# Kernel optimization log

Measured on AMD Instinct MI355X. Metric: run time of the kernel, lower is better.

The kernel has to match this reference:

```python
import jax, jax.numpy as jnp
import numpy as np
import math

D = 256; H = 8; DH = 32; FF = 2048; L = 6; B = 4; S = 1022


def _pe(n, d):
    pos = np.arange(n)[:, None]
    div = np.exp(np.arange(0, d, 2) * (-math.log(10000.0) / d))
    pe = np.zeros((n, d), np.float32)
    pe[:, 0::2] = np.sin(pos * div)
    pe[:, 1::2] = np.cos(pos * div)
    return jnp.asarray(pe)


def _ln(x, g, b):
    mu = x.mean(-1, keepdims=True)
    v = ((x - mu) ** 2).mean(-1, keepdims=True)
    return (x - mu) / jnp.sqrt(v + 1e-5) * g + b


def _forward(x, cls1, cls2, Wqkv, bqkv, Wo, bo, ln1_g, ln1_b, W1, b1, W2, b2, ln2_g, ln2_b, idx, pad):
    n = x.shape[1] + 2  # insert cls1 and cls2 tokens
    h = jnp.stack([jnp.concatenate([cls1, x[i, :idx[i]], cls2, x[i, idx[i]:]], axis=0) for i in range(B)])
    h = h + _pe(n, D)[None]  # [B,N,D]
    # block-diagonal two-segment mask per sample (additive bias form)
    pos = np.arange(n)
    bias = []
    for i in range(B):
        v1 = pos <= idx[i]
        v2 = (pos > idx[i]) & (pos < n - pad[i])
        allowed = np.outer(v1, v1) | np.outer(v2, v2)
        bias.append(np.where(allowed, 0.0, -1e9).astype(np.float32))
    bias = jnp.asarray(np.stack(bias))[:, None]  # [B,1,N,N]
    scale = 1.0 / math.sqrt(DH)
    for l in range(L):
        qkv = h @ Wqkv[l].T + bqkv[l]  # [B,N,3D]
        q, k, v = jnp.split(qkv, 3, axis=-1)
        q = q.reshape(B, n, H, DH).transpose(0, 2, 1, 3)
        k = k.reshape(B, n, H, DH).transpose(0, 2, 1, 3)
        v = v.reshape(B, n, H, DH).transpose(0, 2, 1, 3)
        scores = jnp.einsum('bhqd,bhkd->bhqk', q, k) * scale + bias
        p = jax.nn.softmax(scores, axis=-1)
        a = jnp.einsum('bhqk,bhkd->bhqd', p, v).transpose(0, 2, 1, 3).reshape(B, n, D)
        h = _ln(h + a @ Wo[l].T + bo[l], ln1_g[l], ln1_b[l])
        ff = jax.nn.relu(h @ W1[l].T + b1[l]) @ W2[l].T + b2[l]
        h = _ln(h + ff, ln2_g[l], ln2_b[l])
    # cls token outputs: position 0 (cls1) and position idx+1 (cls2)
    return jnp.stack([jnp.stack([h[i, 0], h[i, idx[i] + 1]]) for i in range(B)])  # [4,2,256]


def setup_inputs():
    key = jax.random.key(0)
    ks = jax.random.split(key, 8)
    s = 0.02
    return {
        'x': jax.random.normal(ks[0], (B, S, D), jnp.float32),
        'mask': jnp.zeros((1,), jnp.bool_),  # unused by the original forward
        'indices': jnp.array([[500, 600, 400, 300], [0, 0, 0, 0]], jnp.int32),
        'cls1': jax.random.uniform(ks[1], (1, D), jnp.float32),
        'cls2': jax.random.uniform(ks[2], (1, D), jnp.float32),
        'Wqkv': jax.random.normal(ks[3], (L, 3 * D, D), jnp.float32) * s,
        'bqkv': jnp.zeros((L, 3 * D), jnp.float32),
        'Wo': jax.random.normal(ks[4], (L, D, D), jnp.float32) * s,
        'bo': jnp.zeros((L, D), jnp.float32),
        'ln1_g': jnp.ones((L, D), jnp.float32),
        'ln1_b': jnp.zeros((L, D), jnp.float32),
        'W1': jax.random.normal(ks[5], (L, FF, D), jnp.float32) * s,
        'b1': jnp.zeros((L, FF), jnp.float32),
        'W2': jax.random.normal(ks[6], (L, D, FF), jnp.float32) * s,
        'b2': jnp.zeros((L, D), jnp.float32),
        'ln2_g': jnp.ones((L, D), jnp.float32),
        'ln2_b': jnp.zeros((L, D), jnp.float32),
    }


def reference(x, mask, indices, cls1, cls2, Wqkv, bqkv, Wo, bo, ln1_g, ln1_b, W1, b1, W2, b2, ln2_g, ln2_b):
    ind = np.asarray(indices)
    idx = [int(t) for t in ind[0]]
    pad = [int(t) for t in ind[1]]
    return _forward(x, cls1, cls2, Wqkv, bqkv, Wo, bo, ln1_g, ln1_b, W1, b1, W2, b2, ln2_g, ln2_b, idx, pad)
```

## Files before the change

### kernel.cpp

```cpp
#include <hip/hip_runtime.h>
#include <hip/hip_bf16.h>
#include <math.h>

typedef __hip_bfloat16 bf16;
typedef short bf16x8 __attribute__((ext_vector_type(8)));
typedef short short4v __attribute__((ext_vector_type(4)));
typedef float f32x4 __attribute__((ext_vector_type(4)));

#define D_MODEL 256
#define NTOK 1024
#define SEQ 1022
#define BATCH 4
#define NLAYER 6

__device__ inline void gload_lds16(const void* g, void* l) {
    __builtin_amdgcn_global_load_lds(
        (const __attribute__((address_space(1))) void*)g,
        (__attribute__((address_space(3))) void*)l, 16, 0, 0);
}

__global__ __launch_bounds__(256) void cast_kernel(
    const float* __restrict__ in, bf16* __restrict__ out, int n)
{
    int i = (blockIdx.x * 256 + threadIdx.x) * 4;
    if (i >= n) return;
    f32x4 v = *(const f32x4*)(in + i);
    out[i + 0] = __float2bfloat16(v[0]);
    out[i + 1] = __float2bfloat16(v[1]);
    out[i + 2] = __float2bfloat16(v[2]);
    out[i + 3] = __float2bfloat16(v[3]);
}

__global__ __launch_bounds__(256) void embed_kernel(
    const float* __restrict__ x, const float* __restrict__ cls1,
    const float* __restrict__ cls2, const int* __restrict__ ind,
    float* __restrict__ h, bf16* __restrict__ hb)
{
    int i = blockIdx.x * 256 + threadIdx.x;
    int d = i & 255;
    int pos = (i >> 8) & 1023;
    int b = i >> 18;
    int idx = ind[b];
    float v;
    if (pos == 0) v = cls1[d];
    else if (pos == idx + 1) v = cls2[d];
    else if (pos <= idx) v = x[(b * SEQ + pos - 1) * D_MODEL + d];
    else v = x[(b * SEQ + pos - 2) * D_MODEL + d];
    int p = d >> 1;
    float freq = expf(-(float)p * (logf(10000.0f) / 128.0f));
    float ang = (float)pos * freq;
    v += (d & 1) ? cosf(ang) : sinf(ang);
    h[i] = v;
    hb[i] = __float2bfloat16(v);
}

template<int MR, int NR, int RELU, int HAS_RES, int WF32, int WBF16, int WVT>
__global__ __launch_bounds__(256) void mfma_gemm(
    const bf16* __restrict__ A, const bf16* __restrict__ W,
    const float* __restrict__ bias, const float* __restrict__ R,
    float* __restrict__ Cf, bf16* __restrict__ Cb, bf16* __restrict__ vTb,
    int M, int N, int K)
{
    constexpr int BM = MR * 32, BN = NR * 32;
    constexpr int ACH = BM * 4;
    constexpr int BCH = BN * 4;
    __shared__ bf16 As[2][BM * 32];
    __shared__ bf16 Bs[2][BN * 32];
    const int ntile = N / BN;
    const int bx = blockIdx.x % ntile, by = blockIdx.x / ntile;
    const int row0 = by * BM, col0 = bx * BN;
    const int tid = threadIdx.x, lane = tid & 63, wave = tid >> 6;
    const int wr = wave >> 1, wc = wave & 1;
    const int l15 = lane & 15, l4 = lane >> 4;

    f32x4 acc[MR][NR];
    #pragma unroll
    for (int m = 0; m < MR; ++m)
        #pragma unroll
        for (int n = 0; n < NR; ++n) acc[m][n] = (f32x4)0.0f;

    const int nk = K / 32;

    auto stage = [&](int buf, int t) {
        const int k0 = t * 32;
        #pragma unroll
        for (int p = 0; p < ACH / 256; ++p) {
            const int cbase = p * 256 + wave * 64;
            const int chunk = cbase + lane;
            const int r = chunk >> 2, c = chunk & 3;
            gload_lds16(A + (size_t)(row0 + r) * K + k0 + c * 8, &As[buf][cbase * 8]);
        }
        #pragma unroll
        for (int p = 0; p < BCH / 256; ++p) {
            const int cbase = p * 256 + wave * 64;
            const int chunk = cbase + lane;
            const int r = chunk >> 2, c = chunk & 3;
            gload_lds16(W + (size_t)(col0 + r) * K + k0 + c * 8, &Bs[buf][cbase * 8]);
        }
    };

    stage(0, 0);
    __syncthreads();
    int cur = 0;
    for (int t = 0; t < nk; ++t) {
        if (t + 1 < nk) stage(cur ^ 1, t + 1);
        bf16x8 af[MR], bfr[NR];
        #pragma unroll
        for (int m = 0; m < MR; ++m)
            af[m] = *(const bf16x8*)&As[cur][(wr * MR * 16 + m * 16 + l15) * 32 + l4 * 8];
        #pragma unroll
        for (int n = 0; n < NR; ++n)
            bfr[n] = *(const bf16x8*)&Bs[cur][(wc * NR * 16 + n * 16 + l15) * 32 + l4 * 8];
        #pragma unroll
        for (int m = 0; m < MR; ++m)
            #pragma unroll
            for (int n = 0; n < NR; ++n)
                acc[m][n] = __builtin_amdgcn_mfma_f32_16x16x32_bf16(af[m], bfr[n], acc[m][n], 0, 0, 0);
        __syncthreads();
        cur ^= 1;
    }

    #pragma unroll
    for (int m = 0; m < MR; ++m) {
        #pragma unroll
        for (int n = 0; n < NR; ++n) {
            const int col = col0 + wc * NR * 16 + n * 16 + l15;
            const float bv = bias[col];
            #pragma unroll
            for (int r = 0; r < 4; ++r) {
                const int row = row0 + wr * MR * 16 + m * 16 + l4 * 4 + r;
                float v = acc[m][n][r] + bv;
                if (HAS_RES) v += R[(size_t)row * N + col];
                if (RELU) v = fmaxf(v, 0.0f);
                if (WF32) Cf[(size_t)row * N + col] = v;
                if (WBF16) {
                    if (WVT && col >= 512) {
                        const int hh = (col >> 5) - 16, d = col & 31;
                        const int bb = row >> 10, tt = row & 1023;
                        vTb[(((size_t)bb * 8 + hh) * 32 + d) * 1024 + tt] = __float2bfloat16(v);
                    } else {
                        Cb[(size_t)row * N + col] = __float2bfloat16(v);
                    }
                }
            }
        }
    }
}

template<int K>
__global__ __launch_bounds__(256) void gemm256_ln_kernel(
    const bf16* __restrict__ A, const bf16* __restrict__ W,
    const float* __restrict__ bias, const float* __restrict__ g,
    const float* __restrict__ be, float* __restrict__ h, bf16* __restrict__ hb)
{
    constexpr int KW = K / 4;
    constexpr int NSTEP = KW / 32;
    __shared__ float part[4][16][260];
    const int tid = threadIdx.x, lane = tid & 63, wave = tid >> 6;
    const int l15 = lane & 15, l4 = lane >> 4;
    const int row0 = blockIdx.x * 16;
    const int kbase = wave * KW;

    f32x4 acc[16];
    #pragma unroll
    for (int n = 0; n < 16; ++n) acc[n] = (f32x4)0.0f;

    #pragma unroll
    for (int s = 0; s < NSTEP; ++s) {
        const int kk = kbase + s * 32;
        const bf16x8 af = *(const bf16x8*)(A + (size_t)(row0 + l15) * K + kk + l4 * 8);
        #pragma unroll
        for (int n = 0; n < 16; ++n) {
            const bf16x8 bf_ = *(const bf16x8*)(W + (size_t)(n * 16 + l15) * K + kk + l4 * 8);
            acc[n] = __builtin_amdgcn_mfma_f32_16x16x32_bf16(af, bf_, acc[n], 0, 0, 0);
        }
    }
    #pragma unroll
    for (int n = 0; n < 16; ++n)
        #pragma unroll
        for (int r = 0; r < 4; ++r)
            part[wave][l4 * 4 + r][n * 16 + l15] = acc[n][r];
    __syncthreads();

    const int row = tid >> 4, colg = tid & 15;
    f32x4 v[4];
    #pragma unroll
    for (int e = 0; e < 4; ++e) {
        v[e] = *(const f32x4*)&part[0][row][colg * 16 + e * 4];
        #pragma unroll
        for (int w = 1; w < 4; ++w)
            v[e] += *(const f32x4*)&part[w][row][colg * 16 + e * 4];
    }
    float* hrow = h + (size_t)(row0 + row) * 256 + colg * 16;
    float s1 = 0.0f;
    #pragma unroll
    for (int e = 0; e < 4; ++e) {
        const f32x4 bv = *(const f32x4*)(bias + colg * 16 + e * 4);
        const f32x4 rv = *(const f32x4*)(hrow + e * 4);
        v[e] += bv + rv;
        s1 += (v[e][0] + v[e][1]) + (v[e][2] + v[e][3]);
    }
    #pragma unroll
    for (int off = 8; off >= 1; off >>= 1) s1 += __shfl_xor(s1, off);
    const float mu = s1 * (1.0f / 256.0f);
    float s2 = 0.0f;
    #pragma unroll
    for (int e = 0; e < 4; ++e) {
        #pragma unroll
        for (int q = 0; q < 4; ++q) { const float d = v[e][q] - mu; s2 += d * d; }
    }
    #pragma unroll
    for (int off = 8; off >= 1; off >>= 1) s2 += __shfl_xor(s2, off);
    const float inv = 1.0f / sqrtf(s2 * (1.0f / 256.0f) + 1e-5f);

    short* hbrow = (short*)hb + (size_t)(row0 + row) * 256 + colg * 16;
    #pragma unroll
    for (int e = 0; e < 4; ++e) {
        const f32x4 gv = *(const f32x4*)(g + colg * 16 + e * 4);
        const f32x4 bv2 = *(const f32x4*)(be + colg * 16 + e * 4);
        f32x4 y;
        short4v pk;
        #pragma unroll
        for (int q = 0; q < 4; ++q) {
            y[q] = (v[e][q] - mu) * inv * gv[q] + bv2[q];
            pk[q] = __builtin_bit_cast(short, __float2bfloat16(y[q]));
        }
        *(f32x4*)(hrow + e * 4) = y;
        *(short4v*)(hbrow + e * 4) = pk;
    }
}

__global__ __launch_bounds__(256) void attn_mfma_kernel(
    const bf16* __restrict__ qkvb, const bf16* __restrict__ vT,
    bf16* __restrict__ att, const int* __restrict__ ind)
{
    __shared__ bf16 Ps[4][16][72];
    const int qt = blockIdx.x & 15;
    const int hh = (blockIdx.x >> 4) & 7;
    const int b  = blockIdx.x >> 7;
    const int idx = ind[b];
    const int segEnd = NTOK - ind[4 + b];
    const int tid = threadIdx.x, lane = tid & 63, wave = tid >> 6;
    const int l15 = lane & 15, l4 = lane >> 4;
    const int q0 = qt * 64 + wave * 16;
    const size_t tokbase = (size_t)b * NTOK;
    const bf16* vTh = vT + (((size_t)b * 8 + hh) * 32) * 1024;
    const float scale = 0.17677669529663687f;

    const bf16x8 qfrag = *(const bf16x8*)(qkvb + (tokbase + q0 + l15) * 768 + hh * 32 + l4 * 8);

    f32x4 acc_o[2];
    acc_o[0] = (f32x4)0.0f; acc_o[1] = (f32x4)0.0f;
    float mrun[4], lrun[4];
    bool v1q[4], v2q[4];
    #pragma unroll
    for (int r = 0; r < 4; ++r) {
        mrun[r] = -1e30f; lrun[r] = 0.0f;
        const int qg = q0 + l4 * 4 + r;
        v1q[r] = (qg <= idx);
        v2q[r] = (qg > idx) && (qg < segEnd);
    }

    const int kbeg = (q0 <= idx) ? 0 : (idx + 1);
    const int kend = (q0 + 15 > idx) ? segEnd : (idx + 1);

    for (int k0 = (kbeg & ~63); k0 < kend; k0 += 64) {
        f32x4 sc[4];
        #pragma unroll
        for (int kt = 0; kt < 4; ++kt) {
            const bf16x8 kf = *(const bf16x8*)
                (qkvb + (tokbase + k0 + kt * 16 + l15) * 768 + 256 + hh * 32 + l4 * 8);
            sc[kt] = __builtin_amdgcn_mfma_f32_16x16x32_bf16(qfrag, kf, (f32x4)0.0f, 0, 0, 0);
        }
        float mloc[4] = {-1e30f, -1e30f, -1e30f, -1e30f};
        #pragma unroll
        for (int kt = 0; kt < 4; ++kt) {
            const int k = k0 + kt * 16 + l15;
            const bool v1k = (k <= idx);
            const bool v2k = (k > idx) && (k < segEnd);
            #pragma unroll
            for (int r = 0; r < 4; ++r) {
                const bool ok = (v1q[r] && v1k) || (v2q[r] && v2k);
                const float s = ok ? sc[kt][r] * scale : -1e30f;
                sc[kt][r] = s;
                mloc[r] = fmaxf(mloc[r], s);
            }
        }
        #pragma unroll
        for (int r = 0; r < 4; ++r) {
            mloc[r] = fmaxf(mloc[r], __shfl_xor(mloc[r], 1));
            mloc[r] = fmaxf(mloc[r], __shfl_xor(mloc[r], 2));
            mloc[r] = fmaxf(mloc[r], __shfl_xor(mloc[r], 4));
            mloc[r] = fmaxf(mloc[r], __shfl_xor(mloc[r], 8));
            const float mnew = fmaxf(mrun[r], mloc[r]);
            const float c = __expf(mrun[r] - mnew);
            mrun[r] = mnew;
            mloc[r] = c;
        }
        float psum[4] = {0.0f, 0.0f, 0.0f, 0.0f};
        #pragma unroll
        for (int kt = 0; kt < 4; ++kt) {
            #pragma unroll
            for (int r = 0; r < 4; ++r) {
                const float s = sc[kt][r];
                const float p = (s > -5e29f) ? __expf(s - mrun[r]) : 0.0f;
                psum[r] += p;
                Ps[wave][l4 * 4 + r][kt * 16 + l15] = __float2bfloat16(p);
            }
        }
        #pragma unroll
        for (int r = 0; r < 4; ++r) {
            float ps = psum[r];
            ps += __shfl_xor(ps, 1); ps += __shfl_xor(ps, 2);
            ps += __shfl_xor(ps, 4); ps += __shfl_xor(ps, 8);
            lrun[r] = lrun[r] * mloc[r] + ps;
            acc_o[0][r] *= mloc[r];
            acc_o[1][r] *= mloc[r];
        }
        #pragma unroll
        for (int ks = 0; ks < 2; ++ks) {
            const bf16x8 pa = *(const bf16x8*)&Ps[wave][l15][ks * 32 + l4 * 8];
            #pragma unroll
            for (int dt = 0; dt < 2; ++dt) {
                const bf16x8 vb = *(const bf16x8*)
                    (vTh + (size_t)(dt * 16 + l15) * 1024 + k0 + ks * 32 + l4 * 8);
                acc_o[dt] = __builtin_amdgcn_mfma_f32_16x16x32_bf16(pa, vb, acc_o[dt], 0, 0, 0);
            }
        }
    }

    #pragma unroll
    for (int r = 0; r < 4; ++r) {
        const float invl = (lrun[r] > 0.0f) ? (1.0f / lrun[r]) : 0.0f;
        const int qg = q0 + l4 * 4 + r;
        bf16* op = att + (tokbase + qg) * 256 + hh * 32 + l15;
        op[0]  = __float2bfloat16(acc_o[0][r] * invl);
        op[16] = __float2bfloat16(acc_o[1][r] * invl);
    }
}

__global__ __launch_bounds__(256) void gather_kernel(
    const float* __restrict__ h, const int* __restrict__ ind, float* __restrict__ out)
{
    int b = blockIdx.x;
    int tid = threadIdx.x;
    out[(b * 2 + 0) * 256 + tid] = h[(b * NTOK + 0) * 256 + tid];
    out[(b * 2 + 1) * 256 + tid] = h[(b * NTOK + ind[b] + 1) * 256 + tid];
}

extern "C" void kernel_launch(void* const* d_in, const int* in_sizes, int n_in,
                              void* d_out, int out_size, void* d_ws, size_t ws_size,
                              hipStream_t stream)
{
    const float* x    = (const float*)d_in[0];
    const int*   ind  = (const int*)d_in[2];
    const float* cls1 = (const float*)d_in[3];
    const float* cls2 = (const float*)d_in[4];
    const float* Wqkv = (const float*)d_in[5];
    const float* bqkv = (const float*)d_in[6];
    const float* Wo   = (const float*)d_in[7];
    const float* bo   = (const float*)d_in[8];
    const float* g1   = (const float*)d_in[9];
    const float* be1  = (const float*)d_in[10];
    const float* W1   = (const float*)d_in[11];
    const float* bf1  = (const float*)d_in[12];
    const float* W2   = (const float*)d_in[13];
    const float* bf2  = (const float*)d_in[14];
    const float* g2   = (const float*)d_in[15];
    const float* be2  = (const float*)d_in[16];
    float* out = (float*)d_out;

    float* ws   = (float*)d_ws;
    float* h    = ws;
    bf16* hb    = (bf16*)(h + 1048576);
    bf16* qkvb  = hb + 1048576;
    bf16* vTb   = qkvb + 3145728;
    bf16* attb  = vTb + 1048576;
    bf16* ffb   = attb + 1048576;
    bf16* wqkvb = ffb + 8388608;
    bf16* wob   = wqkvb + 1179648;
    bf16* w1b   = wob + 393216;
    bf16* w2b   = w1b + 3145728;

    const int M = BATCH * NTOK;

    cast_kernel<<<1152, 256, 0, stream>>>(Wqkv, wqkvb, 1179648);
    cast_kernel<<<384,  256, 0, stream>>>(Wo,   wob,   393216);
    cast_kernel<<<3072, 256, 0, stream>>>(W1,   w1b,   3145728);
    cast_kernel<<<3072, 256, 0, stream>>>(W2,   w2b,   3145728);

    embed_kernel<<<M, 256, 0, stream>>>(x, cls1, cls2, ind, h, hb);

    for (int l = 0; l < NLAYER; ++l) {
        const bf16*  Wqkv_l = wqkvb + (size_t)l * 768 * 256;
        const float* bqkv_l = bqkv + (size_t)l * 768;
        const bf16*  Wo_l   = wob + (size_t)l * 256 * 256;
        const float* bo_l   = bo + (size_t)l * 256;
        const float* g1_l   = g1 + (size_t)l * 256;
        const float* be1_l  = be1 + (size_t)l * 256;
        const bf16*  W1_l   = w1b + (size_t)l * 2048 * 256;
        const float* bf1_l  = bf1 + (size_t)l * 2048;
        const bf16*  W2_l   = w2b + (size_t)l * 256 * 2048;
        const float* bf2_l  = bf2 + (size_t)l * 256;
        const float* g2_l   = g2 + (size_t)l * 256;
        const float* be2_l  = be2 + (size_t)l * 256;

        mfma_gemm<2, 4, 0, 0, 0, 1, 1><<<(M / 64) * (768 / 128), 256, 0, stream>>>(
            hb, Wqkv_l, bqkv_l, nullptr, nullptr, qkvb, vTb, M, 768, 256);
        attn_mfma_kernel<<<BATCH * 8 * 16, 256, 0, stream>>>(qkvb, vTb, attb, ind);
        gemm256_ln_kernel<256><<<M / 16, 256, 0, stream>>>(
            attb, Wo_l, bo_l, g1_l, be1_l, h, hb);
        mfma_gemm<2, 4, 1, 0, 0, 1, 0><<<(M / 64) * (2048 / 128), 256, 0, stream>>>(
            hb, W1_l, bf1_l, nullptr, nullptr, ffb, nullptr, M, 2048, 256);
        gemm256_ln_kernel<2048><<<M / 16, 256, 0, stream>>>(
            ffb, W2_l, bf2_l, g2_l, be2_l, h, hb);
    }

    gather_kernel<<<BATCH, 256, 0, stream>>>(h, ind, out);
}
```

Baseline: 594.1 us.

## Fuse attention with Wo+LN and W2+LN with next-layer QKV projection

Attention now runs one block per 16-query tile covering all 8 heads, with the output kept in LDS and fed straight into the Wo projection, residual and LayerNorm, so the attention buffer no longer round-trips through global memory. The W2 GEMM+LN kernel now uses 512 threads and also computes the next layer's QKV projection from the normalized rows held in LDS, removing a separate launch. The four weight-cast kernels are merged into one launch. In exchange, the attention grid shrinks to 256 blocks and each block rereads the whole Wo tile, which may reduce parallelism.

```diff
diff --git a/kernel.cpp b/kernel.cpp
--- a/kernel.cpp
+++ b/kernel.cpp
@@ -19,16 +19,24 @@
         (__attribute__((address_space(3))) void*)l, 16, 0, 0);
 }
 
-__global__ __launch_bounds__(256) void cast_kernel(
-    const float* __restrict__ in, bf16* __restrict__ out, int n)
-{
-    int i = (blockIdx.x * 256 + threadIdx.x) * 4;
-    if (i >= n) return;
-    f32x4 v = *(const f32x4*)(in + i);
-    out[i + 0] = __float2bfloat16(v[0]);
-    out[i + 1] = __float2bfloat16(v[1]);
-    out[i + 2] = __float2bfloat16(v[2]);
-    out[i + 3] = __float2bfloat16(v[3]);
+__global__ __launch_bounds__(256) void cast4_kernel(
+    const float* __restrict__ s0, bf16* __restrict__ d0,
+    const float* __restrict__ s1, bf16* __restrict__ d1,
+    const float* __restrict__ s2, bf16* __restrict__ d2,
+    const float* __restrict__ s3, bf16* __restrict__ d3)
+{
+    const int bid = blockIdx.x;
+    const float* s; bf16* d; int base;
+    if (bid < 1152)      { s = s0; d = d0; base = bid; }
+    else if (bid < 1536) { s = s1; d = d1; base = bid - 1152; }
+    else if (bid < 4608) { s = s2; d = d2; base = bid - 1536; }
+    else                 { s = s3; d = d3; base = bid - 4608; }
+    const int i = (base * 256 + threadIdx.x) * 4;
+    f32x4 v = *(const f32x4*)(s + i);
+    d[i + 0] = __float2bfloat16(v[0]);
+    d[i + 1] = __float2bfloat16(v[1]);
+    d[i + 2] = __float2bfloat16(v[2]);
+    d[i + 3] = __float2bfloat16(v[3]);
 }
 
 __global__ __launch_bounds__(256) void embed_kernel(
@@ -147,102 +155,22 @@
     }
 }
 
-template<int K>
-__global__ __launch_bounds__(256) void gemm256_ln_kernel(
-    const bf16* __restrict__ A, const bf16* __restrict__ W,
-    const float* __restrict__ bias, const float* __restrict__ g,
-    const float* __restrict__ be, float* __restrict__ h, bf16* __restrict__ hb)
-{
-    constexpr int KW = K / 4;
-    constexpr int NSTEP = KW / 32;
+__global__ __launch_bounds__(512) void attn_wo_ln_kernel(
+    const bf16* __restrict__ qkvb, const bf16* __restrict__ vT,
+    const bf16* __restrict__ Wo, const float* __restrict__ bo,
+    const float* __restrict__ g, const float* __restrict__ be,
+    float* __restrict__ h, bf16* __restrict__ hb, const int* __restrict__ ind)
+{
+    __shared__ bf16 Ps[8][16][72];
+    __shared__ bf16 att_s[16][264];
     __shared__ float part[4][16][260];
-    const int tid = threadIdx.x, lane = tid & 63, wave = tid >> 6;
-    const int l15 = lane & 15, l4 = lane >> 4;
-    const int row0 = blockIdx.x * 16;
-    const int kbase = wave * KW;
-
-    f32x4 acc[16];
-    #pragma unroll
-    for (int n = 0; n < 16; ++n) acc[n] = (f32x4)0.0f;
-
-    #pragma unroll
-    for (int s = 0; s < NSTEP; ++s) {
-        const int kk = kbase + s * 32;
-        const bf16x8 af = *(const bf16x8*)(A + (size_t)(row0 + l15) * K + kk + l4 * 8);
-        #pragma unroll
-        for (int n = 0; n < 16; ++n) {
-            const bf16x8 bf_ = *(const bf16x8*)(W + (size_t)(n * 16 + l15) * K + kk + l4 * 8);
-            acc[n] = __builtin_amdgcn_mfma_f32_16x16x32_bf16(af, bf_, acc[n], 0, 0, 0);
-        }
-    }
-    #pragma unroll
-    for (int n = 0; n < 16; ++n)
-        #pragma unroll
-        for (int r = 0; r < 4; ++r)
-            part[wave][l4 * 4 + r][n * 16 + l15] = acc[n][r];
-    __syncthreads();
-
-    const int row = tid >> 4, colg = tid & 15;
-    f32x4 v[4];
-    #pragma unroll
-    for (int e = 0; e < 4; ++e) {
-        v[e] = *(const f32x4*)&part[0][row][colg * 16 + e * 4];
-        #pragma unroll
-        for (int w = 1; w < 4; ++w)
-            v[e] += *(const f32x4*)&part[w][row][colg * 16 + e * 4];
-    }
-    float* hrow = h + (size_t)(row0 + row) * 256 + colg * 16;
-    float s1 = 0.0f;
-    #pragma unroll
-    for (int e = 0; e < 4; ++e) {
-        const f32x4 bv = *(const f32x4*)(bias + colg * 16 + e * 4);
-        const f32x4 rv = *(const f32x4*)(hrow + e * 4);
-        v[e] += bv + rv;
-        s1 += (v[e][0] + v[e][1]) + (v[e][2] + v[e][3]);
-    }
-    #pragma unroll
-    for (int off = 8; off >= 1; off >>= 1) s1 += __shfl_xor(s1, off);
-    const float mu = s1 * (1.0f / 256.0f);
-    float s2 = 0.0f;
-    #pragma unroll
-    for (int e = 0; e < 4; ++e) {
-        #pragma unroll
-        for (int q = 0; q < 4; ++q) { const float d = v[e][q] - mu; s2 += d * d; }
-    }
-    #pragma unroll
-    for (int off = 8; off >= 1; off >>= 1) s2 += __shfl_xor(s2, off);
-    const float inv = 1.0f / sqrtf(s2 * (1.0f / 256.0f) + 1e-5f);
-
-    short* hbrow = (short*)hb + (size_t)(row0 + row) * 256 + colg * 16;
-    #pragma unroll
-    for (int e = 0; e < 4; ++e) {
-        const f32x4 gv = *(const f32x4*)(g + colg * 16 + e * 4);
-        const f32x4 bv2 = *(const f32x4*)(be + colg * 16 + e * 4);
-        f32x4 y;
-        short4v pk;
-        #pragma unroll
-        for (int q = 0; q < 4; ++q) {
-            y[q] = (v[e][q] - mu) * inv * gv[q] + bv2[q];
-            pk[q] = __builtin_bit_cast(short, __float2bfloat16(y[q]));
-        }
-        *(f32x4*)(hrow + e * 4) = y;
-        *(short4v*)(hbrow + e * 4) = pk;
-    }
-}
-
-__global__ __launch_bounds__(256) void attn_mfma_kernel(
-    const bf16* __restrict__ qkvb, const bf16* __restrict__ vT,
-    bf16* __restrict__ att, const int* __restrict__ ind)
-{
-    __shared__ bf16 Ps[4][16][72];
-    const int qt = blockIdx.x & 15;
-    const int hh = (blockIdx.x >> 4) & 7;
-    const int b  = blockIdx.x >> 7;
+    const int qt = blockIdx.x & 63;
+    const int b  = blockIdx.x >> 6;
     const int idx = ind[b];
     const int segEnd = NTOK - ind[4 + b];
-    const int tid = threadIdx.x, lane = tid & 63, wave = tid >> 6;
+    const int tid = threadIdx.x, lane = tid & 63, hh = tid >> 6;
     const int l15 = lane & 15, l4 = lane >> 4;
-    const int q0 = qt * 64 + wave * 16;
+    const int q0 = qt * 16;
     const size_t tokbase = (size_t)b * NTOK;
     const bf16* vTh = vT + (((size_t)b * 8 + hh) * 32) * 1024;
     const float scale = 0.17677669529663687f;
@@ -305,7 +233,7 @@
                 const float s = sc[kt][r];
                 const float p = (s > -5e29f) ? __expf(s - mrun[r]) : 0.0f;
                 psum[r] += p;
-                Ps[wave][l4 * 4 + r][kt * 16 + l15] = __float2bfloat16(p);
+                Ps[hh][l4 * 4 + r][kt * 16 + l15] = __float2bfloat16(p);
             }
         }
         #pragma unroll
@@ -319,7 +247,7 @@
         }
         #pragma unroll
         for (int ks = 0; ks < 2; ++ks) {
-            const bf16x8 pa = *(const bf16x8*)&Ps[wave][l15][ks * 32 + l4 * 8];
+            const bf16x8 pa = *(const bf16x8*)&Ps[hh][l15][ks * 32 + l4 * 8];
             #pragma unroll
             for (int dt = 0; dt < 2; ++dt) {
                 const bf16x8 vb = *(const bf16x8*)
@@ -332,10 +260,191 @@
     #pragma unroll
     for (int r = 0; r < 4; ++r) {
         const float invl = (lrun[r] > 0.0f) ? (1.0f / lrun[r]) : 0.0f;
-        const int qg = q0 + l4 * 4 + r;
-        bf16* op = att + (tokbase + qg) * 256 + hh * 32 + l15;
-        op[0]  = __float2bfloat16(acc_o[0][r] * invl);
-        op[16] = __float2bfloat16(acc_o[1][r] * invl);
+        att_s[l4 * 4 + r][hh * 32 + l15]      = __float2bfloat16(acc_o[0][r] * invl);
+        att_s[l4 * 4 + r][hh * 32 + 16 + l15] = __float2bfloat16(acc_o[1][r] * invl);
+    }
+    __syncthreads();
+
+    f32x4 wacc[16];
+    #pragma unroll
+    for (int n = 0; n < 16; ++n) wacc[n] = (f32x4)0.0f;
+    {
+        const bf16x8 af = *(const bf16x8*)&att_s[l15][hh * 32 + l4 * 8];
+        #pragma unroll
+        for (int n = 0; n < 16; ++n) {
+            const bf16x8 bfr = *(const bf16x8*)(Wo + (size_t)(n * 16 + l15) * 256 + hh * 32 + l4 * 8);
+            wacc[n] = __builtin_amdgcn_mfma_f32_16x16x32_bf16(af, bfr, wacc[n], 0, 0, 0);
+        }
+    }
+    if (hh < 4) {
+        #pragma unroll
+        for (int n = 0; n < 16; ++n)
+            #pragma unroll
+            for (int r = 0; r < 4; ++r)
+                part[hh][l4 * 4 + r][n * 16 + l15] = wacc[n][r];
+    }
+    __syncthreads();
+    if (hh >= 4) {
+        #pragma unroll
+        for (int n = 0; n < 16; ++n)
+            #pragma unroll
+            for (int r = 0; r < 4; ++r)
+                part[hh - 4][l4 * 4 + r][n * 16 + l15] += wacc[n][r];
+    }
+    __syncthreads();
+
+    const int row = tid >> 5, c8 = (tid & 31) * 8;
+    f32x4 v0, v1;
+    v0 = *(const f32x4*)&part[0][row][c8];
+    v1 = *(const f32x4*)&part[0][row][c8 + 4];
+    #pragma unroll
+    for (int w = 1; w < 4; ++w) {
+        v0 += *(const f32x4*)&part[w][row][c8];
+        v1 += *(const f32x4*)&part[w][row][c8 + 4];
+    }
+    float* hrow = h + (tokbase + q0 + row) * 256 + c8;
+    v0 += *(const f32x4*)(bo + c8)     + *(const f32x4*)(hrow);
+    v1 += *(const f32x4*)(bo + c8 + 4) + *(const f32x4*)(hrow + 4);
+    float s1 = (v0[0] + v0[1]) + (v0[2] + v0[3]) + (v1[0] + v1[1]) + (v1[2] + v1[3]);
+    #pragma unroll
+    for (int off = 16; off >= 1; off >>= 1) s1 += __shfl_xor(s1, off);
+    const float mu = s1 * (1.0f / 256.0f);
+    float s2 = 0.0f;
+    #pragma unroll
+    for (int q = 0; q < 4; ++q) { float d0 = v0[q] - mu, d1 = v1[q] - mu; s2 += d0 * d0 + d1 * d1; }
+    #pragma unroll
+    for (int off = 16; off >= 1; off >>= 1) s2 += __shfl_xor(s2, off);
+    const float inv = 1.0f / sqrtf(s2 * (1.0f / 256.0f) + 1e-5f);
+    short* hbrow = (short*)hb + (tokbase + q0 + row) * 256 + c8;
+    const f32x4 gv0 = *(const f32x4*)(g + c8),  gv1 = *(const f32x4*)(g + c8 + 4);
+    const f32x4 ev0 = *(const f32x4*)(be + c8), ev1 = *(const f32x4*)(be + c8 + 4);
+    f32x4 y0, y1; short4v p0, p1;
+    #pragma unroll
+    for (int q = 0; q < 4; ++q) {
+        y0[q] = (v0[q] - mu) * inv * gv0[q] + ev0[q];
+        y1[q] = (v1[q] - mu) * inv * gv1[q] + ev1[q];
+        p0[q] = __builtin_bit_cast(short, __float2bfloat16(y0[q]));
+        p1[q] = __builtin_bit_cast(short, __float2bfloat16(y1[q]));
+    }
+    *(f32x4*)(hrow) = y0;  *(f32x4*)(hrow + 4) = y1;
+    *(short4v*)(hbrow) = p0;  *(short4v*)(hbrow + 4) = p1;
+}
+
+template<int SKIPQKV>
+__global__ __launch_bounds__(512) void w2ln_qkv_kernel(
+    const bf16* __restrict__ ffb, const bf16* __restrict__ W2,
+    const float* __restrict__ b2, const float* __restrict__ g,
+    const float* __restrict__ be, float* __restrict__ h, bf16* __restrict__ hb,
+    const bf16* __restrict__ Wq, const float* __restrict__ bq,
+    bf16* __restrict__ qkvb, bf16* __restrict__ vTb)
+{
+    __shared__ float part[4][16][260];
+    __shared__ bf16 hbuf[16][264];
+    const int tid = threadIdx.x, lane = tid & 63, wave = tid >> 6;
+    const int l15 = lane & 15, l4 = lane >> 4;
+    const int row0 = blockIdx.x * 16;
+
+    f32x4 acc[16];
+    #pragma unroll
+    for (int n = 0; n < 16; ++n) acc[n] = (f32x4)0.0f;
+    #pragma unroll
+    for (int s = 0; s < 8; ++s) {
+        const int kk = wave * 256 + s * 32;
+        const bf16x8 af = *(const bf16x8*)(ffb + (size_t)(row0 + l15) * 2048 + kk + l4 * 8);
+        #pragma unroll
+        for (int n = 0; n < 16; ++n) {
+            const bf16x8 bfr = *(const bf16x8*)(W2 + (size_t)(n * 16 + l15) * 2048 + kk + l4 * 8);
+            acc[n] = __builtin_amdgcn_mfma_f32_16x16x32_bf16(af, bfr, acc[n], 0, 0, 0);
+        }
+    }
+    if (wave < 4) {
+        #pragma unroll
+        for (int n = 0; n < 16; ++n)
+            #pragma unroll
+            for (int r = 0; r < 4; ++r)
+                part[wave][l4 * 4 + r][n * 16 + l15] = acc[n][r];
+    }
+    __syncthreads();
+    if (wave >= 4) {
+        #pragma unroll
+        for (int n = 0; n < 16; ++n)
+            #pragma unroll
+            for (int r = 0; r < 4; ++r)
+                part[wave - 4][l4 * 4 + r][n * 16 + l15] += acc[n][r];
+    }
+    __syncthreads();
+
+    const int row = tid >> 5, c8 = (tid & 31) * 8;
+    f32x4 v0 = *(const f32x4*)&part[0][row][c8];
+    f32x4 v1 = *(const f32x4*)&part[0][row][c8 + 4];
+    #pragma unroll
+    for (int w = 1; w < 4; ++w) {
+        v0 += *(const f32x4*)&part[w][row][c8];
+        v1 += *(const f32x4*)&part[w][row][c8 + 4];
+    }
+    float* hrow = h + (size_t)(row0 + row) * 256 + c8;
+    v0 += *(const f32x4*)(b2 + c8)     + *(const f32x4*)(hrow);
+    v1 += *(const f32x4*)(b2 + c8 + 4) + *(const f32x4*)(hrow + 4);
+    float s1 = (v0[0] + v0[1]) + (v0[2] + v0[3]) + (v1[0] + v1[1]) + (v1[2] + v1[3]);
+    #pragma unroll
+    for (int off = 16; off >= 1; off >>= 1) s1 += __shfl_xor(s1, off);
+    const float mu = s1 * (1.0f / 256.0f);
+    float s2 = 0.0f;
+    #pragma unroll
+    for (int q = 0; q < 4; ++q) { float d0 = v0[q] - mu, d1 = v1[q] - mu; s2 += d0 * d0 + d1 * d1; }
+    #pragma unroll
+    for (int off = 16; off >= 1; off >>= 1) s2 += __shfl_xor(s2, off);
+    const float inv = 1.0f / sqrtf(s2 * (1.0f / 256.0f) + 1e-5f);
+    short* hbrow = (short*)hb + (size_t)(row0 + row) * 256 + c8;
+    const f32x4 gv0 = *(const f32x4*)(g + c8),  gv1 = *(const f32x4*)(g + c8 + 4);
+    const f32x4 ev0 = *(const f32x4*)(be + c8), ev1 = *(const f32x4*)(be + c8 + 4);
+    f32x4 y0, y1; short4v p0, p1;
+    #pragma unroll
+    for (int q = 0; q < 4; ++q) {
+        y0[q] = (v0[q] - mu) * inv * gv0[q] + ev0[q];
+        y1[q] = (v1[q] - mu) * inv * gv1[q] + ev1[q];
+        p0[q] = __builtin_bit_cast(short, __float2bfloat16(y0[q]));
+        p1[q] = __builtin_bit_cast(short, __float2bfloat16(y1[q]));
+    }
+    *(f32x4*)(hrow) = y0;  *(f32x4*)(hrow + 4) = y1;
+    *(short4v*)(hbrow) = p0;  *(short4v*)(hbrow + 4) = p1;
+    bf16x8 hp;
+    #pragma unroll
+    for (int q = 0; q < 4; ++q) { hp[q] = p0[q]; hp[4 + q] = p1[q]; }
+    *(bf16x8*)&hbuf[row][c8] = hp;
+    __syncthreads();
+
+    if (!SKIPQKV) {
+        f32x4 qa[6];
+        #pragma unroll
+        for (int n = 0; n < 6; ++n) qa[n] = (f32x4)0.0f;
+        #pragma unroll
+        for (int ks = 0; ks < 8; ++ks) {
+            const bf16x8 af = *(const bf16x8*)&hbuf[l15][ks * 32 + l4 * 8];
+            #pragma unroll
+            for (int n = 0; n < 6; ++n) {
+                const bf16x8 bfr = *(const bf16x8*)
+                    (Wq + (size_t)(wave * 96 + n * 16 + l15) * 256 + ks * 32 + l4 * 8);
+                qa[n] = __builtin_amdgcn_mfma_f32_16x16x32_bf16(af, bfr, qa[n], 0, 0, 0);
+            }
+        }
+        #pragma unroll
+        for (int n = 0; n < 6; ++n) {
+            const int col = wave * 96 + n * 16 + l15;
+            const float bv = bq[col];
+            #pragma unroll
+            for (int r = 0; r < 4; ++r) {
+                const int rowg = row0 + l4 * 4 + r;
+                const float v = qa[n][r] + bv;
+                if (col >= 512) {
+                    const int hh2 = (col >> 5) - 16, d = col & 31;
+                    const int bb = rowg >> 10, tt = rowg & 1023;
+                    vTb[(((size_t)bb * 8 + hh2) * 32 + d) * 1024 + tt] = __float2bfloat16(v);
+                } else {
+                    qkvb[(size_t)rowg * 768 + col] = __float2bfloat16(v);
+                }
+            }
+        }
     }
 }
 
@@ -375,8 +484,7 @@
     bf16* hb    = (bf16*)(h + 1048576);
     bf16* qkvb  = hb + 1048576;
     bf16* vTb   = qkvb + 3145728;
-    bf16* attb  = vTb + 1048576;
-    bf16* ffb   = attb + 1048576;
+    bf16* ffb   = vTb + 1048576;
     bf16* wqkvb = ffb + 8388608;
     bf16* wob   = wqkvb + 1179648;
     bf16* w1b   = wob + 393216;
@@ -384,36 +492,37 @@
 
     const int M = BATCH * NTOK;
 
-    cast_kernel<<<1152, 256, 0, stream>>>(Wqkv, wqkvb, 1179648);
-    cast_kernel<<<384,  256, 0, stream>>>(Wo,   wob,   393216);
-    cast_kernel<<<3072, 256, 0, stream>>>(W1,   w1b,   3145728);
-    cast_kernel<<<3072, 256, 0, stream>>>(W2,   w2b,   3145728);
-
+    cast4_kernel<<<7680, 256, 0, stream>>>(Wqkv, wqkvb, Wo, wob, W1, w1b, W2, w2b);
     embed_kernel<<<M, 256, 0, stream>>>(x, cls1, cls2, ind, h, hb);
 
+    mfma_gemm<2, 4, 0, 0, 0, 1, 1><<<(M / 64) * (768 / 128), 256, 0, stream>>>(
+        hb, wqkvb, bqkv, nullptr, nullptr, qkvb, vTb, M, 768, 256);
+
     for (int l = 0; l < NLAYER; ++l) {
-        const bf16*  Wqkv_l = wqkvb + (size_t)l * 768 * 256;
-        const float* bqkv_l = bqkv + (size_t)l * 768;
-        const bf16*  Wo_l   = wob + (size_t)l * 256 * 256;
-        const float* bo_l   = bo + (size_t)l * 256;
-        const float* g1_l   = g1 + (size_t)l * 256;
-        const float* be1_l  = be1 + (size_t)l * 256;
-        const bf16*  W1_l   = w1b + (size_t)l * 2048 * 256;
-        const float* bf1_l  = bf1 + (size_t)l * 2048;
-        const bf16*  W2_l   = w2b + (size_t)l * 256 * 2048;
-        const float* bf2_l  = bf2 + (size_t)l * 256;
-        const float* g2_l   = g2 + (size_t)l * 256;
-        const float* be2_l  = be2 + (size_t)l * 256;
-
-        mfma_gemm<2, 4, 0, 0, 0, 1, 1><<<(M / 64) * (768 / 128), 256, 0, stream>>>(
-            hb, Wqkv_l, bqkv_l, nullptr, nullptr, qkvb, vTb, M, 768, 256);
-        attn_mfma_kernel<<<BATCH * 8 * 16, 256, 0, stream>>>(qkvb, vTb, attb, ind);
-        gemm256_ln_kernel<256><<<M / 16, 256, 0, stream>>>(
-            attb, Wo_l, bo_l, g1_l, be1_l, h, hb);
+        const bf16*  Wo_l  = wob + (size_t)l * 65536;
+        const float* bo_l  = bo + (size_t)l * 256;
+        const float* g1_l  = g1 + (size_t)l * 256;
+        const float* be1_l = be1 + (size_t)l * 256;
+        const bf16*  W1_l  = w1b + (size_t)l * 524288;
+        const float* b1_l  = bf1 + (size_t)l * 2048;
+        const bf16*  W2_l  = w2b + (size_t)l * 524288;
+        const float* b2_l  = bf2 + (size_t)l * 256;
+        const float* g2_l  = g2 + (size_t)l * 256;
+        const float* be2_l = be2 + (size_t)l * 256;
+
+        attn_wo_ln_kernel<<<BATCH * 64, 512, 0, stream>>>(
+            qkvb, vTb, Wo_l, bo_l, g1_l, be1_l, h, hb, ind);
         mfma_gemm<2, 4, 1, 0, 0, 1, 0><<<(M / 64) * (2048 / 128), 256, 0, stream>>>(
-            hb, W1_l, bf1_l, nullptr, nullptr, ffb, nullptr, M, 2048, 256);
-        gemm256_ln_kernel<2048><<<M / 16, 256, 0, stream>>>(
-            ffb, W2_l, bf2_l, g2_l, be2_l, h, hb);
+            hb, W1_l, b1_l, nullptr, nullptr, ffb, nullptr, M, 2048, 256);
+        if (l < NLAYER - 1) {
+            w2ln_qkv_kernel<0><<<M / 16, 512, 0, stream>>>(
+                ffb, W2_l, b2_l, g2_l, be2_l, h, hb,
+                wqkvb + (size_t)(l + 1) * 196608, bqkv + (size_t)(l + 1) * 768, qkvb, vTb);
+        } else {
+            w2ln_qkv_kernel<1><<<M / 16, 512, 0, stream>>>(
+                ffb, W2_l, b2_l, g2_l, be2_l, h, hb,
+                nullptr, nullptr, nullptr, nullptr);
+        }
     }
 
     gather_kernel<<<BATCH, 256, 0, stream>>>(h, ind, out);
```

After: 709.0 us. 1.19x slower.
